# Kernel tuning notes

Measured on AMD Instinct MI355X. Metric: run time of the kernel, lower is better.

## Reference

```python
import jax, jax.numpy as jnp
import numpy as np

N_NODES = 50000
N_EDGES = 800000
CHANNELS = 96
STEPS = 10
ALPHA = 0.1


def setup_inputs() -> dict:
    key = jax.random.key(0)
    k1, k2 = jax.random.split(key)
    x = jax.random.normal(k1, (N_NODES, CHANNELS), dtype=jnp.float32)
    edge_index = jax.random.randint(k2, (2, N_EDGES), 0, N_NODES, dtype=jnp.int64)
    # gamma initialized exactly as the module: [alpha*(1-alpha)^k for k<steps] + [(1-alpha)^steps]
    gamma = jnp.asarray(
        [ALPHA * (1.0 - ALPHA) ** k for k in range(STEPS)] + [(1.0 - ALPHA) ** STEPS],
        dtype=jnp.float32,
    )
    return {"x": x, "edge_index": edge_index, "gamma": gamma}


def reference(x, edge_index, gamma):
    # GPR-GNN propagation: H^(0)=x, H^(k)=D^-1/2 A D^-1/2 H^(k-1); out = sum_k gamma_k H^(k)
    n = x.shape[0]
    src, dst = edge_index[0], edge_index[1]
    deg = jax.ops.segment_sum(jnp.ones((src.shape[0],), x.dtype), dst, num_segments=n)
    dinv = jnp.where(deg > 0, jax.lax.rsqrt(jnp.maximum(deg, 1.0)), 0.0).astype(x.dtype)
    norm = (dinv[src] * dinv[dst])[:, None]  # [E, 1]

    def prop(h):
        # gather from src, scale by symmetric norm, scatter-add into dst
        return jax.ops.segment_sum(h[src] * norm, dst, num_segments=n)

    out = gamma[0] * x
    h = x
    for k in range(STEPS):
        h = prop(h)
        out = out + gamma[k + 1] * h
    return out
```

## Files before the change

### kernel.cpp

```cpp
#include <hip/hip_runtime.h>
#include <hip/hip_fp16.h>

#define N_NODES 50000
#define N_EDGES 800000
#define CH 96
#define C8 12
#define F4 24
#define STEPS 10
#define SENT N_NODES

#define PSTRIDE_BYTES 9600256
#define PSTRIDE_U4    (PSTRIDE_BYTES / 16)


__global__ void count_deg(const int* __restrict__ ei, int* __restrict__ deg, int ne) {
    int t = blockIdx.x * blockDim.x + threadIdx.x;
    int e = t * 4;
    if (e < ne) {
        int4 d4 = *(const int4*)(ei + ne + e);
        if ((unsigned)d4.x < (unsigned)N_NODES) atomicAdd(&deg[d4.x], 1);
        if ((unsigned)d4.y < (unsigned)N_NODES) atomicAdd(&deg[d4.y], 1);
        if ((unsigned)d4.z < (unsigned)N_NODES) atomicAdd(&deg[d4.z], 1);
        if ((unsigned)d4.w < (unsigned)N_NODES) atomicAdd(&deg[d4.w], 1);
    }
}

__global__ void scan1(const int* __restrict__ deg, int* __restrict__ row_ptr,
                      int* __restrict__ partials, float* __restrict__ dinv, int n) {
    __shared__ int sm[256];
    int i = blockIdx.x * 256 + threadIdx.x;
    int v = 0;
    if (i < n) {
        int d = deg[i];
        dinv[i] = (d > 0) ? (1.0f / sqrtf((float)d)) : 0.0f;
        v = (d + 3) & ~3;
    }
    sm[threadIdx.x] = v;
    __syncthreads();
    for (int off = 1; off < 256; off <<= 1) {
        int t = (threadIdx.x >= off) ? sm[threadIdx.x - off] : 0;
        __syncthreads();
        sm[threadIdx.x] += t;
        __syncthreads();
    }
    if (i < n) row_ptr[i + 1] = sm[threadIdx.x];
    if (threadIdx.x == 255) partials[blockIdx.x] = sm[255];
}

__global__ void scan2(int* __restrict__ partials, int nb) {
    __shared__ int sm[256];
    int v = (threadIdx.x < nb) ? partials[threadIdx.x] : 0;
    sm[threadIdx.x] = v;
    __syncthreads();
    for (int off = 1; off < 256; off <<= 1) {
        int t = (threadIdx.x >= off) ? sm[threadIdx.x - off] : 0;
        __syncthreads();
        sm[threadIdx.x] += t;
        __syncthreads();
    }
    if (threadIdx.x < nb) partials[threadIdx.x] = sm[threadIdx.x] - v;
}

__global__ void scan3(int* __restrict__ row_ptr, const int* __restrict__ partials, int n) {
    int i = blockIdx.x * 256 + threadIdx.x;
    if (i < n) row_ptr[i + 1] += partials[blockIdx.x];
    if (i == 0) row_ptr[0] = 0;
}

__global__ void pad_fill(const int* __restrict__ deg, const int* __restrict__ row_ptr,
                         int* __restrict__ csr_src, int n) {
    int i = blockIdx.x * blockDim.x + threadIdx.x;
    if (i < n) {
        int dg = deg[i];
        int dp = (dg + 3) & ~3;
        int base = row_ptr[i];
        for (int j = dg; j < dp; ++j) csr_src[base + j] = SENT;
    }
}

__global__ void fill_csr(const int* __restrict__ ei, const int* __restrict__ row_ptr,
                         int* __restrict__ deg, int* __restrict__ csr_src, int ne) {
    int t = blockIdx.x * blockDim.x + threadIdx.x;
    int e = t * 4;
    if (e < ne) {
        int4 s4 = *(const int4*)(ei + e);
        int4 d4 = *(const int4*)(ei + ne + e);
        #pragma unroll
        for (int j = 0; j < 4; ++j) {
            int s = (j == 0) ? s4.x : (j == 1) ? s4.y : (j == 2) ? s4.z : s4.w;
            int d = (j == 0) ? d4.x : (j == 1) ? d4.y : (j == 2) ? d4.z : d4.w;
            if ((unsigned)d >= (unsigned)N_NODES) continue;
            if ((unsigned)s >= (unsigned)N_NODES) s = SENT;
            int slot = atomicSub(&deg[d], 1) - 1;
            csr_src[row_ptr[d] + slot] = s;
        }
    }
}

__global__ void prescale16(const float* __restrict__ x, const float* __restrict__ dinv,
                           uint4* __restrict__ p0) {
    int g = blockIdx.x * blockDim.x + threadIdx.x;
    if (g >= N_NODES * C8) return;
    int node = g / C8;
    int c8   = g - node * C8;
    float dv = dinv[node];
    float4 x0 = ((const float4*)x)[node * F4 + c8 * 2];
    float4 x1 = ((const float4*)x)[node * F4 + c8 * 2 + 1];
    uint4 q;
    ((__half2*)&q)[0] = __floats2half2_rn(dv * x0.x, dv * x0.y);
    ((__half2*)&q)[1] = __floats2half2_rn(dv * x0.z, dv * x0.w);
    ((__half2*)&q)[2] = __floats2half2_rn(dv * x1.x, dv * x1.y);
    ((__half2*)&q)[3] = __floats2half2_rn(dv * x1.z, dv * x1.w);
    p0[g] = q;
}

__global__ void zero_sent(uint4* __restrict__ p_base, int nbuf) {
    int t = blockIdx.x * blockDim.x + threadIdx.x;
    if (t < nbuf * C8) {
        uint4 z = {0u, 0u, 0u, 0u};
        p_base[(size_t)(t / C8) * PSTRIDE_U4 + (size_t)SENT * C8 + (t % C8)] = z;
    }
}

__device__ inline void acc_add(float* a, uint4 q) {
    const __half2* h = (const __half2*)&q;
    #pragma unroll
    for (int i = 0; i < 4; ++i) {
        float2 f = __half22float2(h[i]);
        a[2 * i]     += f.x;
        a[2 * i + 1] += f.y;
    }
}

__global__ __launch_bounds__(256) void prop16(const uint4* __restrict__ p_in,
                                              uint4* __restrict__ p_out,
                                              float* __restrict__ out,
                                              const float* __restrict__ x,
                                              const int* __restrict__ row_ptr,
                                              const int* __restrict__ csr_src,
                                              const float* __restrict__ dinv,
                                              const float* __restrict__ gamma, int k) {
    int g = blockIdx.x * blockDim.x + threadIdx.x;
    if (g >= N_NODES * C8) return;
    int node = g / C8;
    int c8   = g - node * C8;
    int beg = row_ptr[node];
    int end = row_ptr[node + 1];

    float acc[8] = {0.f, 0.f, 0.f, 0.f, 0.f, 0.f, 0.f, 0.f};

    for (int e = beg; e < end; e += 4) {
        int4 m = *(const int4*)(csr_src + e);
        uint4 q0 = p_in[m.x * C8 + c8];
        uint4 q1 = p_in[m.y * C8 + c8];
        uint4 q2 = p_in[m.z * C8 + c8];
        uint4 q3 = p_in[m.w * C8 + c8];
        acc_add(acc, q0);
        acc_add(acc, q1);
        acc_add(acc, q2);
        acc_add(acc, q3);
    }

    float dv  = dinv[node];
    float dv2 = dv * dv;

    if (p_out) {
        uint4 q;
        ((__half2*)&q)[0] = __floats2half2_rn(dv2 * acc[0], dv2 * acc[1]);
        ((__half2*)&q)[1] = __floats2half2_rn(dv2 * acc[2], dv2 * acc[3]);
        ((__half2*)&q)[2] = __floats2half2_rn(dv2 * acc[4], dv2 * acc[5]);
        ((__half2*)&q)[3] = __floats2half2_rn(dv2 * acc[6], dv2 * acc[7]);
        p_out[g] = q;
    }

    if (out) {
        float gk = gamma[k + 1] * dv;
        int ob = node * F4 + c8 * 2;
        float4 o0, o1;
        if (k == 0) {
            float g0 = gamma[0];
            float4 x0 = ((const float4*)x)[ob];
            float4 x1 = ((const float4*)x)[ob + 1];
            o0.x = fmaf(gk, acc[0], g0 * x0.x); o0.y = fmaf(gk, acc[1], g0 * x0.y);
            o0.z = fmaf(gk, acc[2], g0 * x0.z); o0.w = fmaf(gk, acc[3], g0 * x0.w);
            o1.x = fmaf(gk, acc[4], g0 * x1.x); o1.y = fmaf(gk, acc[5], g0 * x1.y);
            o1.z = fmaf(gk, acc[6], g0 * x1.z); o1.w = fmaf(gk, acc[7], g0 * x1.w);
        } else {
            o0 = ((float4*)out)[ob];
            o1 = ((float4*)out)[ob + 1];
            o0.x = fmaf(gk, acc[0], o0.x); o0.y = fmaf(gk, acc[1], o0.y);
            o0.z = fmaf(gk, acc[2], o0.z); o0.w = fmaf(gk, acc[3], o0.w);
            o1.x = fmaf(gk, acc[4], o1.x); o1.y = fmaf(gk, acc[5], o1.y);
            o1.z = fmaf(gk, acc[6], o1.z); o1.w = fmaf(gk, acc[7], o1.w);
        }
        ((float4*)out)[ob]     = o0;
        ((float4*)out)[ob + 1] = o1;
    }
}

__global__ __launch_bounds__(256) void finalize(const uint4* __restrict__ p_base,
                                                const float* __restrict__ x,
                                                const float* __restrict__ dinv,
                                                const float* __restrict__ gamma,
                                                float* __restrict__ out) {
    int g = blockIdx.x * blockDim.x + threadIdx.x;
    if (g >= N_NODES * C8) return;
    int node = g / C8;
    int c8   = g - node * C8;
    float dv  = dinv[node];
    float rdv = (dv > 0.f) ? (1.f / dv) : 0.f;

    int ob = node * F4 + c8 * 2;
    float g0 = gamma[0];
    float4 x0 = ((const float4*)x)[ob];
    float4 x1 = ((const float4*)x)[ob + 1];
    float o[8] = {g0 * x0.x, g0 * x0.y, g0 * x0.z, g0 * x0.w,
                  g0 * x1.x, g0 * x1.y, g0 * x1.z, g0 * x1.w};

    const uint4* p = p_base + (size_t)PSTRIDE_U4 + g;
    for (int k = 1; k <= STEPS; ++k) {
        uint4 q = *p;
        p += (size_t)PSTRIDE_U4;
        float gk = gamma[k] * rdv;
        const __half2* h = (const __half2*)&q;
        #pragma unroll
        for (int i = 0; i < 4; ++i) {
            float2 f = __half22float2(h[i]);
            o[2 * i]     = fmaf(gk, f.x, o[2 * i]);
            o[2 * i + 1] = fmaf(gk, f.y, o[2 * i + 1]);
        }
    }
    float4 o0 = {o[0], o[1], o[2], o[3]};
    float4 o1 = {o[4], o[5], o[6], o[7]};
    ((float4*)out)[ob]     = o0;
    ((float4*)out)[ob + 1] = o1;
}


static inline size_t align_up(size_t v, size_t a) { return (v + a - 1) & ~(a - 1); }

extern "C" void kernel_launch(void* const* d_in, const int* in_sizes, int n_in,
                              void* d_out, int out_size, void* d_ws, size_t ws_size,
                              hipStream_t stream) {
    const float* x     = (const float*)d_in[0];
    const int*   ei    = (const int*)d_in[1];
    const float* gamma = (const float*)d_in[2];
    float*       out   = (float*)d_out;

    const int n  = N_NODES;
    const int ne = N_EDGES;
    const int nblk_nodes = (n + 255) / 256;
    const int ne_pad_max = ne + 4 * n;

    char*  ws  = (char*)d_ws;
    size_t off = 0;
    int*   deg      = (int*)(ws + off);   off = align_up(off + (size_t)n * 4, 256);
    int*   row_ptr  = (int*)(ws + off);   off = align_up(off + (size_t)(n + 1) * 4, 256);
    int*   partials = (int*)(ws + off);   off = align_up(off + (size_t)nblk_nodes * 4, 256);
    float* dinv     = (float*)(ws + off); off = align_up(off + (size_t)n * 4, 256);
    int*   csr_src  = (int*)(ws + off);   off = align_up(off + (size_t)ne_pad_max * 4, 256);
    uint4* p_base   = (uint4*)(ws + off);

    const bool deferred = (ws_size >= off + 11ull * PSTRIDE_BYTES);
    const int  nbuf     = deferred ? 11 : 2;

    (void)hipMemsetAsync(deg, 0, (size_t)n * 4, stream);

    const int nblk_e4 = (ne / 4 + 255) / 256;
    count_deg<<<nblk_e4, 256, 0, stream>>>(ei, deg, ne);

    scan1<<<nblk_nodes, 256, 0, stream>>>(deg, row_ptr, partials, dinv, n);
    scan2<<<1, 256, 0, stream>>>(partials, nblk_nodes);
    scan3<<<nblk_nodes, 256, 0, stream>>>(row_ptr, partials, n);

    pad_fill<<<nblk_nodes, 256, 0, stream>>>(deg, row_ptr, csr_src, n);
    fill_csr<<<nblk_e4, 256, 0, stream>>>(ei, row_ptr, deg, csr_src, ne);

    const int ng = n * C8;
    const int nblk_g = (ng + 255) / 256;
    prescale16<<<nblk_g, 256, 0, stream>>>(x, dinv, p_base);
    zero_sent<<<1, 256, 0, stream>>>(p_base, nbuf);

    if (deferred) {
        for (int k = 0; k < STEPS; ++k) {
            const uint4* pin  = p_base + (size_t)k * PSTRIDE_U4;
            uint4*       pout = p_base + (size_t)(k + 1) * PSTRIDE_U4;
            prop16<<<nblk_g, 256, 0, stream>>>(pin, pout, nullptr, x,
                                               row_ptr, csr_src, dinv, gamma, k);
        }
        finalize<<<nblk_g, 256, 0, stream>>>(p_base, x, dinv, gamma, out);
    } else {
        uint4* pA = p_base;
        uint4* pB = p_base + (size_t)PSTRIDE_U4;
        const uint4* pin = pA;
        uint4* pout = pB;
        for (int k = 0; k < STEPS; ++k) {
            uint4* pw = (k == STEPS - 1) ? nullptr : pout;
            prop16<<<nblk_g, 256, 0, stream>>>(pin, pw, out, x,
                                               row_ptr, csr_src, dinv, gamma, k);
            pin  = pout;
            pout = (pout == pB) ? pA : pB;
        }
    }
}
```

Before: 434.9 us.

## Slice feature buffers into 8 channel slabs and use 16-bit CSR indices

```diff
diff --git a/kernel.cpp b/kernel.cpp
--- a/kernel.cpp
+++ b/kernel.cpp
@@ -4,13 +4,14 @@
 #define N_NODES 50000
 #define N_EDGES 800000
 #define CH 96
-#define C8 12
-#define F4 24
+#define NSLICE 8
+#define SCH 12
+#define ROWB 32
 #define STEPS 10
 #define SENT N_NODES
 
-#define PSTRIDE_BYTES 9600256
-#define PSTRIDE_U4    (PSTRIDE_BYTES / 16)
+#define SLICE_STRIDE 1600256ull
+#define SLAB        (8ull * SLICE_STRIDE)
 
 
 __global__ void count_deg(const int* __restrict__ ei, int* __restrict__ deg, int ne) {
@@ -68,18 +69,18 @@
 }
 
 __global__ void pad_fill(const int* __restrict__ deg, const int* __restrict__ row_ptr,
-                         int* __restrict__ csr_src, int n) {
+                         unsigned short* __restrict__ cs, int n) {
     int i = blockIdx.x * blockDim.x + threadIdx.x;
     if (i < n) {
         int dg = deg[i];
         int dp = (dg + 3) & ~3;
         int base = row_ptr[i];
-        for (int j = dg; j < dp; ++j) csr_src[base + j] = SENT;
+        for (int j = dg; j < dp; ++j) cs[base + j] = (unsigned short)SENT;
     }
 }
 
 __global__ void fill_csr(const int* __restrict__ ei, const int* __restrict__ row_ptr,
-                         int* __restrict__ deg, int* __restrict__ csr_src, int ne) {
+                         int* __restrict__ deg, unsigned short* __restrict__ cs, int ne) {
     int t = blockIdx.x * blockDim.x + threadIdx.x;
     int e = t * 4;
     if (e < ne) {
@@ -92,148 +93,181 @@
             if ((unsigned)d >= (unsigned)N_NODES) continue;
             if ((unsigned)s >= (unsigned)N_NODES) s = SENT;
             int slot = atomicSub(&deg[d], 1) - 1;
-            csr_src[row_ptr[d] + slot] = s;
-        }
-    }
-}
-
-__global__ void prescale16(const float* __restrict__ x, const float* __restrict__ dinv,
-                           uint4* __restrict__ p0) {
-    int g = blockIdx.x * blockDim.x + threadIdx.x;
-    if (g >= N_NODES * C8) return;
-    int node = g / C8;
-    int c8   = g - node * C8;
+            cs[row_ptr[d] + slot] = (unsigned short)s;
+        }
+    }
+}
+
+__global__ __launch_bounds__(256) void prescale16(const float* __restrict__ x,
+                                                  const float* __restrict__ dinv,
+                                                  char* __restrict__ p0) {
+    int slice = blockIdx.x & 7;
+    int node  = (blockIdx.x >> 3) * 256 + threadIdx.x;
+    if (node >= N_NODES) return;
     float dv = dinv[node];
-    float4 x0 = ((const float4*)x)[node * F4 + c8 * 2];
-    float4 x1 = ((const float4*)x)[node * F4 + c8 * 2 + 1];
-    uint4 q;
-    ((__half2*)&q)[0] = __floats2half2_rn(dv * x0.x, dv * x0.y);
-    ((__half2*)&q)[1] = __floats2half2_rn(dv * x0.z, dv * x0.w);
-    ((__half2*)&q)[2] = __floats2half2_rn(dv * x1.x, dv * x1.y);
-    ((__half2*)&q)[3] = __floats2half2_rn(dv * x1.z, dv * x1.w);
-    p0[g] = q;
-}
-
-__global__ void zero_sent(uint4* __restrict__ p_base, int nbuf) {
+    const float4* xb = (const float4*)((const char*)x + (size_t)node * 384 + slice * 48);
+    float4 x0 = xb[0], x1 = xb[1], x2 = xb[2];
+    uint4 qa; uint2 qb;
+    ((__half2*)&qa)[0] = __floats2half2_rn(dv * x0.x, dv * x0.y);
+    ((__half2*)&qa)[1] = __floats2half2_rn(dv * x0.z, dv * x0.w);
+    ((__half2*)&qa)[2] = __floats2half2_rn(dv * x1.x, dv * x1.y);
+    ((__half2*)&qa)[3] = __floats2half2_rn(dv * x1.z, dv * x1.w);
+    ((__half2*)&qb)[0] = __floats2half2_rn(dv * x2.x, dv * x2.y);
+    ((__half2*)&qb)[1] = __floats2half2_rn(dv * x2.z, dv * x2.w);
+    char* po = p0 + (size_t)slice * SLICE_STRIDE + (size_t)node * ROWB;
+    *(uint4*)po = qa;
+    *(uint2*)(po + 16) = qb;
+}
+
+__global__ void zero_sent(char* __restrict__ p_base, int nbuf) {
     int t = blockIdx.x * blockDim.x + threadIdx.x;
-    if (t < nbuf * C8) {
+    if (t < nbuf * NSLICE) {
+        char* p = p_base + (size_t)(t / NSLICE) * SLAB
+                         + (size_t)(t % NSLICE) * SLICE_STRIDE + (size_t)SENT * ROWB;
         uint4 z = {0u, 0u, 0u, 0u};
-        p_base[(size_t)(t / C8) * PSTRIDE_U4 + (size_t)SENT * C8 + (t % C8)] = z;
-    }
-}
-
-__device__ inline void acc_add(float* a, uint4 q) {
+        *(uint4*)p = z;
+        *(uint2*)(p + 16) = make_uint2(0u, 0u);
+    }
+}
+
+__device__ inline void acc8(float* a, uint4 q) {
     const __half2* h = (const __half2*)&q;
     #pragma unroll
     for (int i = 0; i < 4; ++i) {
         float2 f = __half22float2(h[i]);
-        a[2 * i]     += f.x;
-        a[2 * i + 1] += f.y;
-    }
-}
-
-__global__ __launch_bounds__(256) void prop16(const uint4* __restrict__ p_in,
-                                              uint4* __restrict__ p_out,
+        a[2 * i] += f.x; a[2 * i + 1] += f.y;
+    }
+}
+__device__ inline void acc4(float* a, uint2 q) {
+    const __half2* h = (const __half2*)&q;
+    #pragma unroll
+    for (int i = 0; i < 2; ++i) {
+        float2 f = __half22float2(h[i]);
+        a[2 * i] += f.x; a[2 * i + 1] += f.y;
+    }
+}
+
+__global__ __launch_bounds__(256) void prop16(const char* __restrict__ pin_slab,
+                                              char* __restrict__ pout_slab,
                                               float* __restrict__ out,
                                               const float* __restrict__ x,
                                               const int* __restrict__ row_ptr,
-                                              const int* __restrict__ csr_src,
+                                              const unsigned short* __restrict__ cs,
                                               const float* __restrict__ dinv,
                                               const float* __restrict__ gamma, int k) {
-    int g = blockIdx.x * blockDim.x + threadIdx.x;
-    if (g >= N_NODES * C8) return;
-    int node = g / C8;
-    int c8   = g - node * C8;
+    int slice = blockIdx.x & 7;
+    int node  = (blockIdx.x >> 3) * 256 + threadIdx.x;
+    if (node >= N_NODES) return;
+    const char* pin = pin_slab + (size_t)slice * SLICE_STRIDE;
     int beg = row_ptr[node];
     int end = row_ptr[node + 1];
 
-    float acc[8] = {0.f, 0.f, 0.f, 0.f, 0.f, 0.f, 0.f, 0.f};
+    float acc[12];
+    #pragma unroll
+    for (int i = 0; i < 12; ++i) acc[i] = 0.f;
 
     for (int e = beg; e < end; e += 4) {
-        int4 m = *(const int4*)(csr_src + e);
-        uint4 q0 = p_in[m.x * C8 + c8];
-        uint4 q1 = p_in[m.y * C8 + c8];
-        uint4 q2 = p_in[m.z * C8 + c8];
-        uint4 q3 = p_in[m.w * C8 + c8];
-        acc_add(acc, q0);
-        acc_add(acc, q1);
-        acc_add(acc, q2);
-        acc_add(acc, q3);
-    }
-
-    float dv  = dinv[node];
-    float dv2 = dv * dv;
-
-    if (p_out) {
-        uint4 q;
-        ((__half2*)&q)[0] = __floats2half2_rn(dv2 * acc[0], dv2 * acc[1]);
-        ((__half2*)&q)[1] = __floats2half2_rn(dv2 * acc[2], dv2 * acc[3]);
-        ((__half2*)&q)[2] = __floats2half2_rn(dv2 * acc[4], dv2 * acc[5]);
-        ((__half2*)&q)[3] = __floats2half2_rn(dv2 * acc[6], dv2 * acc[7]);
-        p_out[g] = q;
+        ushort4 m = *(const ushort4*)(cs + e);
+        const char* r0 = pin + (size_t)m.x * ROWB;
+        const char* r1 = pin + (size_t)m.y * ROWB;
+        const char* r2 = pin + (size_t)m.z * ROWB;
+        const char* r3 = pin + (size_t)m.w * ROWB;
+        uint4 a0 = *(const uint4*)r0; uint2 b0 = *(const uint2*)(r0 + 16);
+        uint4 a1 = *(const uint4*)r1; uint2 b1 = *(const uint2*)(r1 + 16);
+        uint4 a2 = *(const uint4*)r2; uint2 b2 = *(const uint2*)(r2 + 16);
+        uint4 a3 = *(const uint4*)r3; uint2 b3 = *(const uint2*)(r3 + 16);
+        acc8(acc, a0); acc4(acc + 8, b0);
+        acc8(acc, a1); acc4(acc + 8, b1);
+        acc8(acc, a2); acc4(acc + 8, b2);
+        acc8(acc, a3); acc4(acc + 8, b3);
+    }
+
+    float dv = dinv[node];
+
+    if (pout_slab) {
+        float s = dv * dv;
+        uint4 qa; uint2 qb;
+        ((__half2*)&qa)[0] = __floats2half2_rn(s * acc[0], s * acc[1]);
+        ((__half2*)&qa)[1] = __floats2half2_rn(s * acc[2], s * acc[3]);
+        ((__half2*)&qa)[2] = __floats2half2_rn(s * acc[4], s * acc[5]);
+        ((__half2*)&qa)[3] = __floats2half2_rn(s * acc[6], s * acc[7]);
+        ((__half2*)&qb)[0] = __floats2half2_rn(s * acc[8], s * acc[9]);
+        ((__half2*)&qb)[1] = __floats2half2_rn(s * acc[10], s * acc[11]);
+        char* po = pout_slab + (size_t)slice * SLICE_STRIDE + (size_t)node * ROWB;
+        *(uint4*)po = qa;
+        *(uint2*)(po + 16) = qb;
     }
 
     if (out) {
         float gk = gamma[k + 1] * dv;
-        int ob = node * F4 + c8 * 2;
-        float4 o0, o1;
+        float4* ob = (float4*)((char*)out + (size_t)node * 384 + slice * 48);
+        float4 o0, o1, o2;
         if (k == 0) {
             float g0 = gamma[0];
-            float4 x0 = ((const float4*)x)[ob];
-            float4 x1 = ((const float4*)x)[ob + 1];
+            const float4* xb = (const float4*)((const char*)x + (size_t)node * 384 + slice * 48);
+            float4 x0 = xb[0], x1 = xb[1], x2 = xb[2];
             o0.x = fmaf(gk, acc[0], g0 * x0.x); o0.y = fmaf(gk, acc[1], g0 * x0.y);
             o0.z = fmaf(gk, acc[2], g0 * x0.z); o0.w = fmaf(gk, acc[3], g0 * x0.w);
             o1.x = fmaf(gk, acc[4], g0 * x1.x); o1.y = fmaf(gk, acc[5], g0 * x1.y);
             o1.z = fmaf(gk, acc[6], g0 * x1.z); o1.w = fmaf(gk, acc[7], g0 * x1.w);
+            o2.x = fmaf(gk, acc[8], g0 * x2.x); o2.y = fmaf(gk, acc[9], g0 * x2.y);
+            o2.z = fmaf(gk, acc[10], g0 * x2.z); o2.w = fmaf(gk, acc[11], g0 * x2.w);
         } else {
-            o0 = ((float4*)out)[ob];
-            o1 = ((float4*)out)[ob + 1];
+            o0 = ob[0]; o1 = ob[1]; o2 = ob[2];
             o0.x = fmaf(gk, acc[0], o0.x); o0.y = fmaf(gk, acc[1], o0.y);
             o0.z = fmaf(gk, acc[2], o0.z); o0.w = fmaf(gk, acc[3], o0.w);
             o1.x = fmaf(gk, acc[4], o1.x); o1.y = fmaf(gk, acc[5], o1.y);
             o1.z = fmaf(gk, acc[6], o1.z); o1.w = fmaf(gk, acc[7], o1.w);
-        }
-        ((float4*)out)[ob]     = o0;
-        ((float4*)out)[ob + 1] = o1;
-    }
-}
-
-__global__ __launch_bounds__(256) void finalize(const uint4* __restrict__ p_base,
+            o2.x = fmaf(gk, acc[8], o2.x); o2.y = fmaf(gk, acc[9], o2.y);
+            o2.z = fmaf(gk, acc[10], o2.z); o2.w = fmaf(gk, acc[11], o2.w);
+        }
+        ob[0] = o0; ob[1] = o1; ob[2] = o2;
+    }
+}
+
+__global__ __launch_bounds__(256) void finalize(const char* __restrict__ p_base,
                                                 const float* __restrict__ x,
                                                 const float* __restrict__ dinv,
                                                 const float* __restrict__ gamma,
                                                 float* __restrict__ out) {
-    int g = blockIdx.x * blockDim.x + threadIdx.x;
-    if (g >= N_NODES * C8) return;
-    int node = g / C8;
-    int c8   = g - node * C8;
+    int slice = blockIdx.x & 7;
+    int node  = (blockIdx.x >> 3) * 256 + threadIdx.x;
+    if (node >= N_NODES) return;
     float dv  = dinv[node];
     float rdv = (dv > 0.f) ? (1.f / dv) : 0.f;
 
-    int ob = node * F4 + c8 * 2;
+    const float4* xb = (const float4*)((const char*)x + (size_t)node * 384 + slice * 48);
+    float4 x0 = xb[0], x1 = xb[1], x2 = xb[2];
     float g0 = gamma[0];
-    float4 x0 = ((const float4*)x)[ob];
-    float4 x1 = ((const float4*)x)[ob + 1];
-    float o[8] = {g0 * x0.x, g0 * x0.y, g0 * x0.z, g0 * x0.w,
-                  g0 * x1.x, g0 * x1.y, g0 * x1.z, g0 * x1.w};
-
-    const uint4* p = p_base + (size_t)PSTRIDE_U4 + g;
+    float o[12] = {g0 * x0.x, g0 * x0.y, g0 * x0.z, g0 * x0.w,
+                   g0 * x1.x, g0 * x1.y, g0 * x1.z, g0 * x1.w,
+                   g0 * x2.x, g0 * x2.y, g0 * x2.z, g0 * x2.w};
+
+    const char* p = p_base + SLAB + (size_t)slice * SLICE_STRIDE + (size_t)node * ROWB;
     for (int k = 1; k <= STEPS; ++k) {
-        uint4 q = *p;
-        p += (size_t)PSTRIDE_U4;
+        uint4 qa = *(const uint4*)p;
+        uint2 qb = *(const uint2*)(p + 16);
+        p += SLAB;
         float gk = gamma[k] * rdv;
-        const __half2* h = (const __half2*)&q;
+        const __half2* h = (const __half2*)&qa;
         #pragma unroll
         for (int i = 0; i < 4; ++i) {
             float2 f = __half22float2(h[i]);
             o[2 * i]     = fmaf(gk, f.x, o[2 * i]);
             o[2 * i + 1] = fmaf(gk, f.y, o[2 * i + 1]);
         }
-    }
-    float4 o0 = {o[0], o[1], o[2], o[3]};
-    float4 o1 = {o[4], o[5], o[6], o[7]};
-    ((float4*)out)[ob]     = o0;
-    ((float4*)out)[ob + 1] = o1;
+        const __half2* h2 = (const __half2*)&qb;
+        #pragma unroll
+        for (int i = 0; i < 2; ++i) {
+            float2 f = __half22float2(h2[i]);
+            o[8 + 2 * i] = fmaf(gk, f.x, o[8 + 2 * i]);
+            o[9 + 2 * i] = fmaf(gk, f.y, o[9 + 2 * i]);
+        }
+    }
+    float4* ob = (float4*)((char*)out + (size_t)node * 384 + slice * 48);
+    ob[0] = make_float4(o[0], o[1], o[2], o[3]);
+    ob[1] = make_float4(o[4], o[5], o[6], o[7]);
+    ob[2] = make_float4(o[8], o[9], o[10], o[11]);
 }
 
 
@@ -258,10 +292,11 @@
     int*   row_ptr  = (int*)(ws + off);   off = align_up(off + (size_t)(n + 1) * 4, 256);
     int*   partials = (int*)(ws + off);   off = align_up(off + (size_t)nblk_nodes * 4, 256);
     float* dinv     = (float*)(ws + off); off = align_up(off + (size_t)n * 4, 256);
-    int*   csr_src  = (int*)(ws + off);   off = align_up(off + (size_t)ne_pad_max * 4, 256);
-    uint4* p_base   = (uint4*)(ws + off);
-
-    const bool deferred = (ws_size >= off + 11ull * PSTRIDE_BYTES);
+    unsigned short* cs = (unsigned short*)(ws + off);
+    off = align_up(off + (size_t)ne_pad_max * 2, 256);
+    char*  p_base   = ws + off;
+
+    const bool deferred = (ws_size >= off + 11ull * SLAB);
     const int  nbuf     = deferred ? 11 : 2;
 
     (void)hipMemsetAsync(deg, 0, (size_t)n * 4, stream);
@@ -273,31 +308,30 @@
     scan2<<<1, 256, 0, stream>>>(partials, nblk_nodes);
     scan3<<<nblk_nodes, 256, 0, stream>>>(row_ptr, partials, n);
 
-    pad_fill<<<nblk_nodes, 256, 0, stream>>>(deg, row_ptr, csr_src, n);
-    fill_csr<<<nblk_e4, 256, 0, stream>>>(ei, row_ptr, deg, csr_src, ne);
-
-    const int ng = n * C8;
-    const int nblk_g = (ng + 255) / 256;
-    prescale16<<<nblk_g, 256, 0, stream>>>(x, dinv, p_base);
+    pad_fill<<<nblk_nodes, 256, 0, stream>>>(deg, row_ptr, cs, n);
+    fill_csr<<<nblk_e4, 256, 0, stream>>>(ei, row_ptr, deg, cs, ne);
+
+    const int nblk_sl = NSLICE * nblk_nodes;
+    prescale16<<<nblk_sl, 256, 0, stream>>>(x, dinv, p_base);
     zero_sent<<<1, 256, 0, stream>>>(p_base, nbuf);
 
     if (deferred) {
         for (int k = 0; k < STEPS; ++k) {
-            const uint4* pin  = p_base + (size_t)k * PSTRIDE_U4;
-            uint4*       pout = p_base + (size_t)(k + 1) * PSTRIDE_U4;
-            prop16<<<nblk_g, 256, 0, stream>>>(pin, pout, nullptr, x,
-                                               row_ptr, csr_src, dinv, gamma, k);
-        }
-        finalize<<<nblk_g, 256, 0, stream>>>(p_base, x, dinv, gamma, out);
+            const char* pin  = p_base + (size_t)k * SLAB;
+            char*       pout = p_base + (size_t)(k + 1) * SLAB;
+            prop16<<<nblk_sl, 256, 0, stream>>>(pin, pout, nullptr, x,
+                                                row_ptr, cs, dinv, gamma, k);
+        }
+        finalize<<<nblk_sl, 256, 0, stream>>>(p_base, x, dinv, gamma, out);
     } else {
-        uint4* pA = p_base;
-        uint4* pB = p_base + (size_t)PSTRIDE_U4;
-        const uint4* pin = pA;
-        uint4* pout = pB;
+        char* pA = p_base;
+        char* pB = p_base + SLAB;
+        const char* pin = pA;
+        char* pout = pB;
         for (int k = 0; k < STEPS; ++k) {
-            uint4* pw = (k == STEPS - 1) ? nullptr : pout;
-            prop16<<<nblk_g, 256, 0, stream>>>(pin, pw, out, x,
-                                               row_ptr, csr_src, dinv, gamma, k);
+            char* pw = (k == STEPS - 1) ? nullptr : pout;
+            prop16<<<nblk_sl, 256, 0, stream>>>(pin, pw, out, x,
+                                                row_ptr, cs, dinv, gamma, k);
             pin  = pout;
             pout = (pout == pB) ? pA : pB;
         }
```

New measurement: 706.7 us. +62.5%, slower.
